# Optimization experiments

Hardware: AMD Instinct MI355X
Metric: run time of the kernel (lower is better)

## Reference

```python
import jax, jax.numpy as jnp
import numpy as np

N = 60000      # num_nodes
R = 70         # num_relations
B = 30         # num_bases
E = 1920000    # num_edges (avg degree 32)
STD = 0.1


def setup_inputs() -> dict:
    key = jax.random.key(0)
    ks = jax.random.split(key, 14)
    p = lambda k, shape: (jax.random.normal(k, shape, jnp.float32) * STD)
    inp = {}
    inp['edge_index'] = jax.random.randint(ks[0], (2, E), 0, N, dtype=jnp.int32)
    inp['edge_type'] = jax.random.randint(ks[1], (E,), 0, R, dtype=jnp.int32)
    # layer 1: in=N (identity features), out=32
    inp['att1'] = p(ks[2], (R, B))
    inp['basis1'] = p(ks[3], (B, N, 32))
    inp['root1'] = p(ks[4], (N, 32))
    inp['bias1'] = jnp.zeros((32,), jnp.float32)
    # layer 2: in=32, out=8
    inp['att2'] = p(ks[5], (R, B))
    inp['basis2'] = p(ks[6], (B, 32, 8))
    inp['root2'] = p(ks[7], (32, 8))
    inp['bias2'] = jnp.zeros((8,), jnp.float32)
    # layer 3: in=8, out=1
    inp['att3'] = p(ks[8], (R, B))
    inp['basis3'] = p(ks[9], (B, 8, 1))
    inp['root3'] = p(ks[10], (8, 1))
    inp['bias3'] = jnp.zeros((1,), jnp.float32)
    return inp


def _scatter_mean(msg, dst, num_nodes):
    s = jax.ops.segment_sum(msg, dst, num_segments=num_nodes)          # [N, O]
    cnt = jax.ops.segment_sum(jnp.ones((msg.shape[0], 1), msg.dtype), dst,
                              num_segments=num_nodes)                   # [N, 1]
    return s / jnp.maximum(cnt, 1.0)


def _rgcn(x, edge_index, edge_type, att, basis, root, bias, num_nodes):
    # basis decomposition: weight[r] = sum_b att[r,b] * basis[b]
    weight = jnp.einsum('rb,bio->rio', att, basis)  # [R, in, out]
    src, dst = edge_index[0], edge_index[1]
    if x is None:
        # identity input features -> message is a row of the relation weight
        msg = weight[edge_type, src]                # [E, out]
        self_term = root                            # x @ root with x = I
    else:
        # compute per-relation transforms once, then gather per edge
        h = jnp.einsum('ni,rio->rno', x, weight)    # [R, N, out]
        msg = h[edge_type, src]                     # [E, out]
        self_term = x @ root                        # [N, out]
    aggr = _scatter_mean(msg, dst, num_nodes)       # mean aggregation (old PyG RGCNConv)
    return aggr + self_term + bias


def reference(edge_index, edge_type, att1, basis1, root1, bias1,
              att2, basis2, root2, bias2, att3, basis3, root3, bias3):
    x = jax.nn.relu(_rgcn(None, edge_index, edge_type, att1, basis1, root1, bias1, N))
    x = jax.nn.relu(_rgcn(x, edge_index, edge_type, att2, basis2, root2, bias2, N))
    x = _rgcn(x, edge_index, edge_type, att3, basis3, root3, bias3, N)
    return x  # [N, 1]
```

## Files before the change

### kernel.cpp

```cpp
#include <hip/hip_runtime.h>
#include <hip/hip_bf16.h>
#include <hip/hip_fp16.h>

#define NNODES 60000
#define NREL   70
#define NB     30
#define NEDGE  1920000
#define NBLK   235
#define W2P    320


__global__ void hist2_kernel(const int* __restrict__ src, const int* __restrict__ dst,
                             int* __restrict__ cntS, int* __restrict__ cntD,
                             int* __restrict__ ranks) {
    int e = blockIdx.x * blockDim.x + threadIdx.x;
    if (e < NEDGE) {
        int rS = atomicAdd(&cntS[src[e]], 1);
        int rD = atomicAdd(&cntD[dst[e]], 1);
        ranks[e] = (rD << 16) | rS;
    }
}

__global__ void scanA2_kernel(const int* __restrict__ cntS, const int* __restrict__ cntD,
                              int* __restrict__ bsum) {
    __shared__ int lds[256];
    int half = (blockIdx.x >= NBLK) ? 1 : 0;
    int blk  = blockIdx.x - half * NBLK;
    const int* cnt = half ? cntD : cntS;
    int i = blk * 256 + threadIdx.x;
    int v = (i < NNODES) ? cnt[i] : 0;
    lds[threadIdx.x] = v;
    __syncthreads();
    for (int d = 128; d > 0; d >>= 1) {
        if (threadIdx.x < d) lds[threadIdx.x] += lds[threadIdx.x + d];
        __syncthreads();
    }
    if (threadIdx.x == 0) bsum[half * 256 + blk] = lds[0];
}

__global__ void scanB2_kernel(const int* __restrict__ bsum, int* __restrict__ boff) {
    __shared__ int lds[256];
    for (int half = 0; half < 2; ++half) {
        int v = (threadIdx.x < NBLK) ? bsum[half * 256 + threadIdx.x] : 0;
        lds[threadIdx.x] = v;
        __syncthreads();
        for (int d = 1; d < 256; d <<= 1) {
            int t = (threadIdx.x >= d) ? lds[threadIdx.x - d] : 0;
            __syncthreads();
            lds[threadIdx.x] += t;
            __syncthreads();
        }
        boff[half * 256 + threadIdx.x] = lds[threadIdx.x] - v;
        __syncthreads();
    }
}

__global__ void scanC2_kernel(const int* __restrict__ cntS, const int* __restrict__ cntD,
                              const int* __restrict__ boff,
                              int* __restrict__ offsS, int* __restrict__ offsD) {
    __shared__ int lds[256];
    int half = (blockIdx.x >= NBLK) ? 1 : 0;
    int blk  = blockIdx.x - half * NBLK;
    const int* cnt = half ? cntD : cntS;
    int* offs = half ? offsD : offsS;
    int i = blk * 256 + threadIdx.x;
    int v = (i < NNODES) ? cnt[i] : 0;
    lds[threadIdx.x] = v;
    __syncthreads();
    for (int d = 1; d < 256; d <<= 1) {
        int t = (threadIdx.x >= d) ? lds[threadIdx.x - d] : 0;
        __syncthreads();
        lds[threadIdx.x] += t;
        __syncthreads();
    }
    if (i < NNODES) offs[i] = boff[half * 256 + blk] + lds[threadIdx.x] - v;
}

__global__ void fill2_stream_kernel(const int* __restrict__ src, const int* __restrict__ dst,
                                    const int* __restrict__ et, const int* __restrict__ ranks,
                                    const int* __restrict__ offsS, const int* __restrict__ offsD,
                                    int2* __restrict__ ebufSD) {
    int e = blockIdx.x * blockDim.x + threadIdx.x;
    if (e < NEDGE) {
        int s = src[e], d = dst[e], t = et[e];
        int r = ranks[e];
        int spos = offsS[s] + (r & 0xFFFF);
        int slot = offsD[d] + (r >> 16);
        ebufSD[spos] = make_int2((t << 25) | slot, (t << 16) | d);
    }
}

__global__ void fill2_atomic_kernel(const int* __restrict__ src, const int* __restrict__ dst,
                                    const int* __restrict__ et, const int* __restrict__ ranks,
                                    const int* __restrict__ offsS, const int* __restrict__ offsD,
                                    int* __restrict__ ebufS, int* __restrict__ ebufD) {
    int e = blockIdx.x * blockDim.x + threadIdx.x;
    if (e < NEDGE) {
        int s = src[e], d = dst[e], t = et[e];
        int r = ranks[e];
        ebufD[offsD[d] + (r >> 16)]   = (t << 16) | s;
        ebufS[offsS[s] + (r & 0xFFFF)] = (t << 16) | d;
    }
}


__global__ void wexpand2_kernel(const float* __restrict__ att, const float* __restrict__ basis,
                                float* __restrict__ w2t) {
    int idx = blockIdx.x * blockDim.x + threadIdx.x;
    if (idx >= NREL * 256) return;
    int r = idx >> 8, t = idx & 255, o = t >> 5, i = t & 31;
    float s = 0.f;
    #pragma unroll
    for (int b = 0; b < NB; ++b) s += att[r * NB + b] * basis[b * 256 + i * 8 + o];
    w2t[r * 256 + o * 32 + i] = s;
}

__global__ void wexpand2h_kernel(const float* __restrict__ att, const float* __restrict__ basis,
                                 unsigned short* __restrict__ w2h) {
    int idx = blockIdx.x * blockDim.x + threadIdx.x;
    if (idx >= NREL * W2P) return;
    int r = idx / W2P, t = idx - r * W2P;
    int o = t / 40, i = t - o * 40;
    float s = 0.f;
    if (i < 32) {
        #pragma unroll
        for (int b = 0; b < NB; ++b) s += att[r * NB + b] * basis[b * 256 + i * 8 + o];
    }
    w2h[idx] = __half_as_ushort(__float2half_rn(s));
}

__global__ void wexpand3_kernel(const float* __restrict__ att, const float* __restrict__ basis,
                                float* __restrict__ w3) {
    int idx = blockIdx.x * blockDim.x + threadIdx.x;
    if (idx >= NREL * 8) return;
    int r = idx >> 3, i = idx & 7;
    float s = 0.f;
    #pragma unroll
    for (int b = 0; b < NB; ++b) s += att[r * NB + b] * basis[b * 8 + i];
    w3[idx] = s;
}


__global__ void layer1_scatter_stream_kernel(const int2* __restrict__ ebufSD,
                                             const int* __restrict__ offsS,
                                             const int* __restrict__ cntS,
                                             const float* __restrict__ att1,
                                             const float* __restrict__ basis1,
                                             unsigned short* __restrict__ msgh) {
    __shared__ float att_lds[NREL * 32];
    for (int i = threadIdx.x; i < NREL * 32; i += 256) {
        int r = i >> 5, b = i & 31;
        att_lds[i] = (b < NB) ? att1[r * NB + b] : 0.f;
    }
    __syncthreads();
    int wave = threadIdx.x >> 6, lane = threadIdx.x & 63;
    int s = blockIdx.x * 4 + wave;
    int o = lane & 31, half = lane >> 5;
    int off = offsS[s], c = cntS[s];
    if (c == 0) return;
    float B[32];
    const float* bp = basis1 + (size_t)s * 32 + o;
    #pragma unroll
    for (int b = 0; b < NB; ++b) B[b] = bp[(size_t)b * (NNODES * 32)];
    B[30] = 0.f; B[31] = 0.f;
    for (int k = half; k < c; k += 2) {
        unsigned p = (unsigned)ebufSD[off + k].x;
        int slot = p & 0x01FFFFFF;
        int et   = p >> 25;
        const float4* ar4 = (const float4*)(att_lds + et * 32);
        float m0 = 0.f, m1 = 0.f, m2 = 0.f, m3 = 0.f;
        #pragma unroll
        for (int q = 0; q < 8; ++q) {
            float4 a4 = ar4[q];
            m0 = fmaf(a4.x, B[4 * q + 0], m0);
            m1 = fmaf(a4.y, B[4 * q + 1], m1);
            m2 = fmaf(a4.z, B[4 * q + 2], m2);
            m3 = fmaf(a4.w, B[4 * q + 3], m3);
        }
        float m = (m0 + m1) + (m2 + m3);
        float mo = __shfl_xor(m, 1);
        if ((o & 1) == 0) {
            __half2 h;
            h.x = __float2half_rn(m);
            h.y = __float2half_rn(mo);
            *reinterpret_cast<__half2*>(msgh + (size_t)slot * 32 + o) = h;
        }
    }
}

__global__ void layer1_reduce_kernel(const unsigned short* __restrict__ msgh,
                                     const int* __restrict__ offsD, const int* __restrict__ cntD,
                                     const float* __restrict__ root1,
                                     const float* __restrict__ bias1,
                                     float* __restrict__ x1) {
    int wave = threadIdx.x >> 6, lane = threadIdx.x & 63;
    int n = blockIdx.x * 4 + wave;
    int o2 = (lane & 15) * 2, grp = lane >> 4;
    int off = offsD[n], c = cntD[n];
    float acc0 = 0.f, acc1 = 0.f;
    for (int k = grp; k < c; k += 4) {
        __half2 h = *reinterpret_cast<const __half2*>(msgh + (size_t)(off + k) * 32 + o2);
        float2 f = __half22float2(h);
        acc0 += f.x; acc1 += f.y;
    }
    acc0 += __shfl_xor(acc0, 16); acc0 += __shfl_xor(acc0, 32);
    acc1 += __shfl_xor(acc1, 16); acc1 += __shfl_xor(acc1, 32);
    if (grp == 0) {
        float inv = 1.0f / fmaxf((float)c, 1.0f);
        size_t base = (size_t)n * 32 + o2;
        x1[base]     = fmaxf(acc0 * inv + root1[base]     + bias1[o2],     0.f);
        x1[base + 1] = fmaxf(acc1 * inv + root1[base + 1] + bias1[o2 + 1], 0.f);
    }
}


__global__ void layer1_scatter_kernel(const int* __restrict__ ebufS, const int* __restrict__ offsS,
                                      const int* __restrict__ cntS, const float* __restrict__ att1,
                                      const float* __restrict__ basis1, float* __restrict__ x1acc) {
    int wave = threadIdx.x >> 6, lane = threadIdx.x & 63;
    int s = blockIdx.x * 4 + wave;
    int o = lane & 31, half = lane >> 5;
    int off = offsS[s], c = cntS[s];
    if (c == 0) return;
    float B[NB];
    const float* bp = basis1 + (size_t)s * 32 + o;
    #pragma unroll
    for (int b = 0; b < NB; ++b) B[b] = bp[(size_t)b * (NNODES * 32)];
    for (int k = half; k < c; k += 2) {
        int p  = ebufS[off + k];
        int d  = p & 0xFFFF, et = p >> 16;
        float attv = (o < NB) ? att1[et * NB + o] : 0.f;
        float m = 0.f;
        #pragma unroll
        for (int b = 0; b < NB; ++b) {
            float a = __shfl(attv, (lane & 32) + b);
            m = fmaf(a, B[b], m);
        }
        atomicAdd(&x1acc[(size_t)d * 32 + o], m);
    }
}

__global__ void layer1_finalize_kernel(const int* __restrict__ cntD,
                                       const float* __restrict__ root1,
                                       const float* __restrict__ bias1,
                                       float* __restrict__ x1) {
    int i = blockIdx.x * 256 + threadIdx.x;
    if (i >= NNODES * 32) return;
    int n = i >> 5, o = i & 31;
    float c = (float)cntD[n];
    float v = x1[i] / fmaxf(c, 1.0f) + root1[i] + bias1[o];
    x1[i] = fmaxf(v, 0.0f);
}


__global__ void layer2_src_atomic_kernel(const int2* __restrict__ ebufSD,
                                         const int* __restrict__ offsS, const int* __restrict__ cntS,
                                         const float* __restrict__ x1,
                                         const unsigned short* __restrict__ w2h,
                                         float* __restrict__ x2acc) {
    __shared__ unsigned short w2l[NREL * W2P];
    for (int i = threadIdx.x; i < NREL * W2P; i += 256) w2l[i] = w2h[i];
    __syncthreads();
    int wave = threadIdx.x >> 6, lane = threadIdx.x & 63;
    int s = blockIdx.x * 4 + wave;
    int o = lane & 7, grp = lane >> 3;
    int off = offsS[s], c = cntS[s];
    if (c == 0) return;
    float2 xf[16];
    const float2* xp2 = (const float2*)(x1 + (size_t)s * 32);
    #pragma unroll
    for (int i = 0; i < 16; ++i) xf[i] = xp2[i];
    for (int k0 = 0; k0 < c; k0 += 8) {
        int kk = k0 + grp;
        if (kk < c) {
            int p = ebufSD[off + kk].y;
            int d = p & 0xFFFF, et = p >> 16;
            const unsigned short* wp = w2l + et * W2P + o * 40;
            float a0 = 0.f, a1 = 0.f, a2 = 0.f, a3 = 0.f;
            #pragma unroll
            for (int q = 0; q < 4; ++q) {
                uint4 wv = *reinterpret_cast<const uint4*>(wp + q * 8);
                __half2 h; float2 f;
                h = *reinterpret_cast<const __half2*>(&wv.x); f = __half22float2(h);
                a0 = fmaf(xf[q * 4 + 0].x, f.x, a0); a0 = fmaf(xf[q * 4 + 0].y, f.y, a0);
                h = *reinterpret_cast<const __half2*>(&wv.y); f = __half22float2(h);
                a1 = fmaf(xf[q * 4 + 1].x, f.x, a1); a1 = fmaf(xf[q * 4 + 1].y, f.y, a1);
                h = *reinterpret_cast<const __half2*>(&wv.z); f = __half22float2(h);
                a2 = fmaf(xf[q * 4 + 2].x, f.x, a2); a2 = fmaf(xf[q * 4 + 2].y, f.y, a2);
                h = *reinterpret_cast<const __half2*>(&wv.w); f = __half22float2(h);
                a3 = fmaf(xf[q * 4 + 3].x, f.x, a3); a3 = fmaf(xf[q * 4 + 3].y, f.y, a3);
            }
            float acc = (a0 + a1) + (a2 + a3);
            atomicAdd(&x2acc[(size_t)d * 8 + o], acc);
        }
    }
}

__global__ void layer2_finalize_kernel(const int* __restrict__ cntD,
                                       const float* __restrict__ x1,
                                       const float* __restrict__ root2,
                                       const float* __restrict__ bias2,
                                       float* __restrict__ x2) {
    int t = blockIdx.x * 256 + threadIdx.x;
    if (t >= NNODES * 8) return;
    int n = t >> 3, o = t & 7;
    float self = 0.f;
    const float* xn = x1 + (size_t)n * 32;
    #pragma unroll
    for (int i = 0; i < 32; ++i) self = fmaf(xn[i], root2[i * 8 + o], self);
    float c = (float)cntD[n];
    float v = x2[t] / fmaxf(c, 1.0f) + self + bias2[o];
    x2[t] = fmaxf(v, 0.0f);
}


__global__ void layer3_src_atomic_kernel(const int2* __restrict__ ebufSD,
                                         const int* __restrict__ offsS, const int* __restrict__ cntS,
                                         const float* __restrict__ x2, const float* __restrict__ w3,
                                         float* __restrict__ outacc) {
    __shared__ float w3l[NREL * 8];
    for (int i = threadIdx.x; i < NREL * 8; i += 256) w3l[i] = w3[i];
    __syncthreads();
    int wave = threadIdx.x >> 6, lane = threadIdx.x & 63;
    int s = blockIdx.x * 4 + wave;
    int off = offsS[s], c = cntS[s];
    if (c == 0) return;
    const float4* xp = (const float4*)(x2 + (size_t)s * 8);
    float4 a0 = xp[0], a1 = xp[1];
    for (int k = lane; k < c; k += 64) {
        int p = ebufSD[off + k].y;
        int d = p & 0xFFFF, et = p >> 16;
        const float4* wp = (const float4*)(w3l + et * 8);
        float4 b0 = wp[0], b1 = wp[1];
        float m = a0.x * b0.x + a0.y * b0.y + a0.z * b0.z + a0.w * b0.w
                + a1.x * b1.x + a1.y * b1.y + a1.z * b1.z + a1.w * b1.w;
        atomicAdd(&outacc[d], m);
    }
}

__global__ void layer3_finalize_kernel(const int* __restrict__ cntD,
                                       const float* __restrict__ x2,
                                       const float* __restrict__ root3,
                                       const float* __restrict__ bias3,
                                       float* __restrict__ out) {
    int n = blockIdx.x * 256 + threadIdx.x;
    if (n >= NNODES) return;
    float self = 0.f;
    const float* xn = x2 + (size_t)n * 8;
    #pragma unroll
    for (int i = 0; i < 8; ++i) self = fmaf(xn[i], root3[i], self);
    float c = (float)cntD[n];
    out[n] = out[n] / fmaxf(c, 1.0f) + self + bias3[0];
}


__global__ void layer2_kernel(const int* __restrict__ ebufD, const int* __restrict__ offsD,
                              const int* __restrict__ cntD,
                              const float* __restrict__ x1, const float* __restrict__ w2t,
                              const float* __restrict__ root2, const float* __restrict__ bias2,
                              float* __restrict__ x2) {
    int wave = threadIdx.x >> 6, lane = threadIdx.x & 63;
    int n = blockIdx.x * 4 + wave;
    int o = lane & 7, slot = lane >> 3;
    int off = offsD[n], c = cntD[n];
    float acc = 0.f;
    for (int k0 = 0; k0 < c; k0 += 8) {
        int kk = k0 + slot;
        if (kk < c) {
            int packed = ebufD[off + kk];
            int src = packed & 0xFFFF, et = packed >> 16;
            const float4* xp = (const float4*)(x1 + (size_t)src * 32);
            const float4* wp = (const float4*)(w2t + et * 256 + o * 32);
            #pragma unroll
            for (int i = 0; i < 8; ++i) {
                float4 xv = xp[i], wv = wp[i];
                acc += xv.x * wv.x + xv.y * wv.y + xv.z * wv.z + xv.w * wv.w;
            }
        }
    }
    #pragma unroll
    for (int d = 8; d < 64; d <<= 1) acc += __shfl_xor(acc, d);
    if (lane < 8) {
        float self = 0.f;
        const float* xn = x1 + (size_t)n * 32;
        #pragma unroll
        for (int i = 0; i < 32; ++i) self += xn[i] * root2[i * 8 + o];
        float v = acc / fmaxf((float)c, 1.0f) + self + bias2[o];
        x2[(size_t)n * 8 + o] = fmaxf(v, 0.0f);
    }
}

__global__ void layer3_kernel(const int* __restrict__ ebufD, const int* __restrict__ offsD,
                              const int* __restrict__ cntD,
                              const float* __restrict__ x2, const float* __restrict__ w3,
                              const float* __restrict__ root3, const float* __restrict__ bias3,
                              float* __restrict__ out) {
    int wave = threadIdx.x >> 6, lane = threadIdx.x & 63;
    int n = blockIdx.x * 4 + wave;
    int off = offsD[n], c = cntD[n];
    float acc = 0.f;
    for (int k = lane; k < c; k += 64) {
        int packed = ebufD[off + k];
        int src = packed & 0xFFFF, et = packed >> 16;
        const float4* xp = (const float4*)(x2 + src * 8);
        const float4* wp = (const float4*)(w3 + et * 8);
        float4 a0 = xp[0], a1 = xp[1], b0 = wp[0], b1 = wp[1];
        acc += a0.x * b0.x + a0.y * b0.y + a0.z * b0.z + a0.w * b0.w
             + a1.x * b1.x + a1.y * b1.y + a1.z * b1.z + a1.w * b1.w;
    }
    #pragma unroll
    for (int d = 1; d < 64; d <<= 1) acc += __shfl_xor(acc, d);
    if (lane == 0) {
        float self = 0.f;
        const float* xn = x2 + (size_t)n * 8;
        #pragma unroll
        for (int i = 0; i < 8; ++i) self += xn[i] * root3[i];
        out[n] = acc / fmaxf((float)c, 1.0f) + self + bias3[0];
    }
}


extern "C" void kernel_launch(void* const* d_in, const int* in_sizes, int n_in,
                              void* d_out, int out_size, void* d_ws, size_t ws_size,
                              hipStream_t stream) {
    const int*   edge_index = (const int*)  d_in[0];
    const int*   edge_type  = (const int*)  d_in[1];
    const float* att1   = (const float*) d_in[2];
    const float* basis1 = (const float*) d_in[3];
    const float* root1  = (const float*) d_in[4];
    const float* bias1  = (const float*) d_in[5];
    const float* att2   = (const float*) d_in[6];
    const float* basis2 = (const float*) d_in[7];
    const float* root2  = (const float*) d_in[8];
    const float* bias2  = (const float*) d_in[9];
    const float* att3   = (const float*) d_in[10];
    const float* basis3 = (const float*) d_in[11];
    const float* root3  = (const float*) d_in[12];
    const float* bias3  = (const float*) d_in[13];
    float* out = (float*)d_out;

    const int* srcArr = edge_index;
    const int* dstArr = edge_index + NEDGE;

    char* ws = (char*)d_ws;
    int*   cntS   = (int*)(ws + 0);
    int*   cntD   = (int*)(ws + 240128);
    int*   offsS  = (int*)(ws + 480256);
    int*   offsD  = (int*)(ws + 720384);
    int*   bsum   = (int*)(ws + 960512);
    int*   boff   = (int*)(ws + 962560);
    int*   ebufS  = (int*)(ws + 1442816);
    int*   ebufD  = (int*)(ws + 9122816);
    int2*  ebufSD = (int2*)(ws + 1442816);
    float* w2t    = (float*)(ws + 16802816);
    float* w3     = (float*)(ws + 16874496);
    unsigned short* w2h = (unsigned short*)(ws + 16876800);
    float* x1     = (float*)(ws + 16921600);
    int*   ranks  = (int*)(ws + 16921600);
    float* x2     = (float*)(ws + 24601600);
    unsigned short* msgh = (unsigned short*)(ws + 26521600);
    const bool use_stream = ws_size >= 149401600ULL;

    hipMemsetAsync(ws, 0, 480128, stream);
    hipMemsetAsync((void*)x2, 0, 1920000, stream);
    hipMemsetAsync(d_out, 0, NNODES * 4, stream);

    hist2_kernel<<<NEDGE / 256, 256, 0, stream>>>(srcArr, dstArr, cntS, cntD, ranks);
    scanA2_kernel<<<2 * NBLK, 256, 0, stream>>>(cntS, cntD, bsum);
    scanB2_kernel<<<1, 256, 0, stream>>>(bsum, boff);
    scanC2_kernel<<<2 * NBLK, 256, 0, stream>>>(cntS, cntD, boff, offsS, offsD);
    if (use_stream) {
        fill2_stream_kernel<<<NEDGE / 256, 256, 0, stream>>>(srcArr, dstArr, edge_type, ranks,
                                                             offsS, offsD, ebufSD);
    } else {
        fill2_atomic_kernel<<<NEDGE / 256, 256, 0, stream>>>(srcArr, dstArr, edge_type, ranks,
                                                             offsS, offsD, ebufS, ebufD);
    }

    wexpand2h_kernel<<<(NREL * W2P + 255) / 256, 256, 0, stream>>>(att2, basis2, w2h);
    wexpand3_kernel<<<(NREL * 8 + 255) / 256, 256, 0, stream>>>(att3, basis3, w3);
    if (!use_stream) {
        wexpand2_kernel<<<(NREL * 256 + 255) / 256, 256, 0, stream>>>(att2, basis2, w2t);
    }

    if (use_stream) {
        layer1_scatter_stream_kernel<<<NNODES / 4, 256, 0, stream>>>(ebufSD, offsS, cntS,
                                                                     att1, basis1, msgh);
        layer1_reduce_kernel<<<NNODES / 4, 256, 0, stream>>>(msgh, offsD, cntD, root1, bias1, x1);
    } else {
        hipMemsetAsync((void*)x1, 0, 7680000, stream);
        layer1_scatter_kernel<<<NNODES / 4, 256, 0, stream>>>(ebufS, offsS, cntS, att1, basis1, x1);
        layer1_finalize_kernel<<<(NNODES * 32) / 256, 256, 0, stream>>>(cntD, root1, bias1, x1);
    }

    if (use_stream) {
        layer2_src_atomic_kernel<<<NNODES / 4, 256, 0, stream>>>(ebufSD, offsS, cntS, x1, w2h, x2);
        layer2_finalize_kernel<<<(NNODES * 8 + 255) / 256, 256, 0, stream>>>(cntD, x1, root2, bias2, x2);
        layer3_src_atomic_kernel<<<NNODES / 4, 256, 0, stream>>>(ebufSD, offsS, cntS, x2, w3, out);
        layer3_finalize_kernel<<<(NNODES + 255) / 256, 256, 0, stream>>>(cntD, x2, root3, bias3, out);
    } else {
        layer2_kernel<<<NNODES / 4, 256, 0, stream>>>(ebufD, offsD, cntD, x1, w2t, root2, bias2, x2);
        layer3_kernel<<<NNODES / 4, 256, 0, stream>>>(ebufD, offsD, cntD, x2, w3, root3, bias3, out);
    }
}
```

Baseline: 687.4 us.

## Widen layer1 scatter to float2 per lane, pad LDS rows, enlarge layer2 blocks

The layer1 scatter now has each lane compute two output columns from float2 basis loads, with four edges in flight per wave. This removes the cross-lane shuffle and the half-idle store, and att rows in LDS are padded to 36 floats, likely to reduce bank conflicts. The layer2 weight table stride is padded to 328 halves, and the layer2 kernel uses 1024-thread blocks so the LDS weight copy is shared by 16 waves instead of 4. Costs are twice as many basis registers per lane and lower occupancy from the larger blocks. The workspace offsets are shifted to fit the bigger weight table.

```diff
diff --git a/kernel.cpp b/kernel.cpp
--- a/kernel.cpp
+++ b/kernel.cpp
@@ -7,7 +7,7 @@
 #define NB     30
 #define NEDGE  1920000
 #define NBLK   235
-#define W2P    320
+#define W2P    328
 
 
 __global__ void hist2_kernel(const int* __restrict__ src, const int* __restrict__ dst,
@@ -122,7 +122,7 @@
     int r = idx / W2P, t = idx - r * W2P;
     int o = t / 40, i = t - o * 40;
     float s = 0.f;
-    if (i < 32) {
+    if (o < 8 && i < 32) {
         #pragma unroll
         for (int b = 0; b < NB; ++b) s += att[r * NB + b] * basis[b * 256 + i * 8 + o];
     }
@@ -147,44 +147,41 @@
                                              const float* __restrict__ att1,
                                              const float* __restrict__ basis1,
                                              unsigned short* __restrict__ msgh) {
-    __shared__ float att_lds[NREL * 32];
-    for (int i = threadIdx.x; i < NREL * 32; i += 256) {
-        int r = i >> 5, b = i & 31;
+    __shared__ float att_lds[NREL * 36];
+    for (int i = threadIdx.x; i < NREL * 36; i += 256) {
+        int r = i / 36, b = i - r * 36;
         att_lds[i] = (b < NB) ? att1[r * NB + b] : 0.f;
     }
     __syncthreads();
     int wave = threadIdx.x >> 6, lane = threadIdx.x & 63;
     int s = blockIdx.x * 4 + wave;
-    int o = lane & 31, half = lane >> 5;
+    int o2 = (lane & 15) * 2, quarter = lane >> 4;
     int off = offsS[s], c = cntS[s];
     if (c == 0) return;
-    float B[32];
-    const float* bp = basis1 + (size_t)s * 32 + o;
-    #pragma unroll
-    for (int b = 0; b < NB; ++b) B[b] = bp[(size_t)b * (NNODES * 32)];
-    B[30] = 0.f; B[31] = 0.f;
-    for (int k = half; k < c; k += 2) {
+    float2 B2[32];
+    const float* bp = basis1 + (size_t)s * 32 + o2;
+    #pragma unroll
+    for (int b = 0; b < NB; ++b)
+        B2[b] = *reinterpret_cast<const float2*>(bp + (size_t)b * (NNODES * 32));
+    B2[30] = make_float2(0.f, 0.f); B2[31] = make_float2(0.f, 0.f);
+    for (int k = quarter; k < c; k += 4) {
         unsigned p = (unsigned)ebufSD[off + k].x;
         int slot = p & 0x01FFFFFF;
         int et   = p >> 25;
-        const float4* ar4 = (const float4*)(att_lds + et * 32);
-        float m0 = 0.f, m1 = 0.f, m2 = 0.f, m3 = 0.f;
+        const float4* ar4 = (const float4*)(att_lds + et * 36);
+        float x0 = 0.f, x1p = 0.f, y0 = 0.f, y1p = 0.f;
         #pragma unroll
         for (int q = 0; q < 8; ++q) {
             float4 a4 = ar4[q];
-            m0 = fmaf(a4.x, B[4 * q + 0], m0);
-            m1 = fmaf(a4.y, B[4 * q + 1], m1);
-            m2 = fmaf(a4.z, B[4 * q + 2], m2);
-            m3 = fmaf(a4.w, B[4 * q + 3], m3);
+            x0  = fmaf(a4.x, B2[4 * q + 0].x, x0);  y0  = fmaf(a4.x, B2[4 * q + 0].y, y0);
+            x1p = fmaf(a4.y, B2[4 * q + 1].x, x1p); y1p = fmaf(a4.y, B2[4 * q + 1].y, y1p);
+            x0  = fmaf(a4.z, B2[4 * q + 2].x, x0);  y0  = fmaf(a4.z, B2[4 * q + 2].y, y0);
+            x1p = fmaf(a4.w, B2[4 * q + 3].x, x1p); y1p = fmaf(a4.w, B2[4 * q + 3].y, y1p);
         }
-        float m = (m0 + m1) + (m2 + m3);
-        float mo = __shfl_xor(m, 1);
-        if ((o & 1) == 0) {
-            __half2 h;
-            h.x = __float2half_rn(m);
-            h.y = __float2half_rn(mo);
-            *reinterpret_cast<__half2*>(msgh + (size_t)slot * 32 + o) = h;
-        }
+        __half2 h;
+        h.x = __float2half_rn(x0 + x1p);
+        h.y = __float2half_rn(y0 + y1p);
+        *reinterpret_cast<__half2*>(msgh + (size_t)slot * 32 + o2) = h;
     }
 }
 
@@ -259,10 +256,10 @@
                                          const unsigned short* __restrict__ w2h,
                                          float* __restrict__ x2acc) {
     __shared__ unsigned short w2l[NREL * W2P];
-    for (int i = threadIdx.x; i < NREL * W2P; i += 256) w2l[i] = w2h[i];
+    for (int i = threadIdx.x; i < NREL * W2P; i += 1024) w2l[i] = w2h[i];
     __syncthreads();
     int wave = threadIdx.x >> 6, lane = threadIdx.x & 63;
-    int s = blockIdx.x * 4 + wave;
+    int s = blockIdx.x * 16 + wave;
     int o = lane & 7, grp = lane >> 3;
     int off = offsS[s], c = cntS[s];
     if (c == 0) return;
@@ -455,11 +452,11 @@
     float* w2t    = (float*)(ws + 16802816);
     float* w3     = (float*)(ws + 16874496);
     unsigned short* w2h = (unsigned short*)(ws + 16876800);
-    float* x1     = (float*)(ws + 16921600);
-    int*   ranks  = (int*)(ws + 16921600);
-    float* x2     = (float*)(ws + 24601600);
-    unsigned short* msgh = (unsigned short*)(ws + 26521600);
-    const bool use_stream = ws_size >= 149401600ULL;
+    float* x1     = (float*)(ws + 16923648);
+    int*   ranks  = (int*)(ws + 16923648);
+    float* x2     = (float*)(ws + 24603648);
+    unsigned short* msgh = (unsigned short*)(ws + 26523648);
+    const bool use_stream = ws_size >= 149403648ULL;
 
     hipMemsetAsync(ws, 0, 480128, stream);
     hipMemsetAsync((void*)x2, 0, 1920000, stream);
@@ -494,7 +491,7 @@
     }
 
     if (use_stream) {
-        layer2_src_atomic_kernel<<<NNODES / 4, 256, 0, stream>>>(ebufSD, offsS, cntS, x1, w2h, x2);
+        layer2_src_atomic_kernel<<<NNODES / 16, 1024, 0, stream>>>(ebufSD, offsS, cntS, x1, w2h, x2);
         layer2_finalize_kernel<<<(NNODES * 8 + 255) / 256, 256, 0, stream>>>(cntD, x1, root2, bias2, x2);
         layer3_src_atomic_kernel<<<NNODES / 4, 256, 0, stream>>>(ebufSD, offsS, cntS, x2, w3, out);
         layer3_finalize_kernel<<<(NNODES + 255) / 256, 256, 0, stream>>>(cntD, x2, root3, bias3, out);
```

Result: no change. 697.1 us (+1.4%).
